# Kernel optimization log

Measured on AMD Instinct MI355X. Metric: run time of the kernel, lower is better.

Reference implementation:

```python
import jax, jax.numpy as jnp
import numpy as np

B, S, D = 32, 257, 1024
H, HD = 16, 64
E, R, K = 8, 16, 2
SCALE = HD ** -0.5


def _lora_linear(x, w_fixed, A_all, B_all, bias, idx, gates):
    # x: [B,S,D]; w_fixed: [O,D]; A_all: [E,R,D]; B_all: [E,O,R]; idx: [B,K]; gates: [B,K]
    base = jnp.einsum('bsd,od->bso', x, w_fixed)
    A_sel = A_all[idx]  # [B,K,R,D] per-sample expert gather
    B_sel = B_all[idx]  # [B,K,O,R]
    xa = jnp.einsum('bsd,bkrd->bksr', x, A_sel)          # low-rank down-proj
    expert = jnp.einsum('bksr,bkor,bk->bso', xa, B_sel, gates)
    return base + expert + bias


def setup_inputs() -> dict:
    key = jax.random.key(0)
    ks = jax.random.split(key, 20)
    inp = {
        'hidden_states': jax.random.normal(ks[0], (B, S, D), jnp.float32),
        'top_k_indices': jax.random.randint(ks[1], (B, K), 0, E),
        'top_k_gates': jax.random.uniform(ks[2], (B, K), jnp.float32),
    }
    i = 3
    for name in ('q', 'k', 'v', 'o'):
        inp[f'w{name}_fixed'] = jax.random.normal(ks[i], (D, D), jnp.float32) * 0.02; i += 1
        inp[f'A_{name}'] = jax.random.normal(ks[i], (E, R, D), jnp.float32) * 0.02; i += 1
        inp[f'B_{name}'] = jax.random.normal(ks[i], (E, D, R), jnp.float32) * 0.02; i += 1
        inp[f'b_{name}'] = jnp.zeros((D,), jnp.float32)
    return inp


def reference(hidden_states, top_k_indices, top_k_gates,
              wq_fixed, A_q, B_q, b_q,
              wk_fixed, A_k, B_k, b_k,
              wv_fixed, A_v, B_v, b_v,
              wo_fixed, A_o, B_o, b_o):
    idx, gates = top_k_indices, top_k_gates
    q = _lora_linear(hidden_states, wq_fixed, A_q, B_q, b_q, idx, gates) * SCALE
    k = _lora_linear(hidden_states, wk_fixed, A_k, B_k, b_k, idx, gates)
    v = _lora_linear(hidden_states, wv_fixed, A_v, B_v, b_v, idx, gates)
    # [B,S,D] -> [B,H,S,HD]
    q = q.reshape(B, S, H, HD).transpose(0, 2, 1, 3)
    k = k.reshape(B, S, H, HD).transpose(0, 2, 1, 3)
    v = v.reshape(B, S, H, HD).transpose(0, 2, 1, 3)
    attn = jax.nn.softmax(jnp.einsum('bhsd,bhtd->bhst', q, k), axis=-1)
    out = jnp.einsum('bhst,bhtd->bhsd', attn, v)
    out = out.transpose(0, 2, 1, 3).reshape(B, S, D)
    return _lora_linear(out, wo_fixed, A_o, B_o, b_o, idx, gates)
```

## Files before the change

### kernel.cpp

```cpp
#include <hip/hip_runtime.h>


#define BB 32
#define SS 257
#define DD 1024
#define HH 16
#define HDIM 64
#define EE 8
#define RR 16
#define MTOT (BB * SS)
#define MPAD 8320
#define VTS 264

typedef __attribute__((ext_vector_type(8))) _Float16 f16x8;
typedef __attribute__((ext_vector_type(4))) float f32x4;

static __device__ __forceinline__ float4 ld4(const float* p) {
    return *(const float4*)p;
}
static __device__ __forceinline__ unsigned short f16b(float x) {
    union { _Float16 f; unsigned short u; } cv;
    cv.f = (_Float16)x;
    return cv.u;
}

static __device__ __forceinline__ void gl_lds16(const unsigned short* g,
                                                unsigned short* l) {
    __builtin_amdgcn_global_load_lds(
        (const __attribute__((address_space(1))) unsigned int*)g,
        (__attribute__((address_space(3))) unsigned int*)l, 16, 0, 0);
}

__global__ __launch_bounds__(256) void prep(
    const float* __restrict__ hidden, const float* __restrict__ wq,
    const float* __restrict__ wk, const float* __restrict__ wv,
    const float* __restrict__ wo, const float* __restrict__ Aq,
    const float* __restrict__ Ak, const float* __restrict__ Av,
    const float* __restrict__ Ao, const float* __restrict__ Bq,
    const float* __restrict__ Bk, const float* __restrict__ Bv,
    const float* __restrict__ Bo, const int* __restrict__ tki,
    const float* __restrict__ tkg, unsigned short* __restrict__ Xf,
    unsigned short* __restrict__ Wcat, unsigned short* __restrict__ Who,
    unsigned short* __restrict__ A3, unsigned short* __restrict__ Ao16,
    unsigned short* __restrict__ Bccat, unsigned short* __restrict__ Bco)
{
    const int tid = threadIdx.x;
    int bx = blockIdx.x;
    if (bx < 8320) {
        long i = ((long)bx * 256 + tid) * 4;
        float4 v = (i < (long)MTOT * DD) ? ld4(&hidden[i])
                                         : make_float4(0.f, 0.f, 0.f, 0.f);
        ushort4 hv;
        hv.x = f16b(v.x); hv.y = f16b(v.y); hv.z = f16b(v.z); hv.w = f16b(v.w);
        *(ushort4*)&Xf[i] = hv;
        return;
    }
    bx -= 8320;
    if (bx < 4096) {
        const int sel = bx >> 10;
        long i = ((long)(bx & 1023) * 256 + tid) * 4;
        const float* src = (sel == 0) ? wq : (sel == 1) ? wk
                                          : (sel == 2) ? wv : wo;
        unsigned short* dst =
            (sel < 3) ? Wcat + (size_t)sel * DD * DD : Who;
        float4 v = ld4(&src[i]);
        ushort4 hv;
        hv.x = f16b(v.x); hv.y = f16b(v.y); hv.z = f16b(v.z); hv.w = f16b(v.w);
        *(ushort4*)&dst[i] = hv;
        return;
    }
    bx -= 4096;
    if (bx < 512) {
        const int sel = bx >> 7;
        long i = ((long)(bx & 127) * 256 + tid) * 4;
        const float* src = (sel == 0) ? Aq : (sel == 1) ? Ak
                                          : (sel == 2) ? Av : Ao;
        unsigned short* dst =
            (sel < 3) ? A3 + (size_t)sel * EE * RR * DD : Ao16;
        float4 v = ld4(&src[i]);
        ushort4 hv;
        hv.x = f16b(v.x); hv.y = f16b(v.y); hv.z = f16b(v.z); hv.w = f16b(v.w);
        *(ushort4*)&dst[i] = hv;
        return;
    }
    bx -= 512;
    {
        const int set = bx >> 8;
        const int i = (bx & 255) * 256 + tid;
        const int b = i >> 11;
        const int rem = i & 2047;
        const int n = rem >> 1;
        const int ke = rem & 1;
        const float* Ball = (set == 0) ? Bq : (set == 1) ? Bk
                                           : (set == 2) ? Bv : Bo;
        const int e = tki[b * 2 + ke];
        const float g = tkg[b * 2 + ke];
        const float* sp = &Ball[((size_t)e * DD + n) * RR];
        unsigned short o16[16];
#pragma unroll
        for (int r4 = 0; r4 < 4; ++r4) {
            float4 v = ld4(sp + r4 * 4);
            o16[r4 * 4 + 0] = f16b(g * v.x);
            o16[r4 * 4 + 1] = f16b(g * v.y);
            o16[r4 * 4 + 2] = f16b(g * v.z);
            o16[r4 * 4 + 3] = f16b(g * v.w);
        }
        unsigned short* dst =
            (set < 3) ? &Bccat[((size_t)b * 3072 + set * 1024 + n) * 32 + ke * 16]
                      : &Bco[((size_t)b * 1024 + n) * 32 + ke * 16];
        *(uint4*)&dst[0] = *(uint4*)&o16[0];
        *(uint4*)&dst[8] = *(uint4*)&o16[8];
    }
}

#define COMPUTE1()                                                             \
    do {                                                                       \
        f16x8 af[4], bf[4];                                                    \
        const int sb = (quad ^ ((l16 >> 1) & 3)) * 8;                          \
        _Pragma("unroll") for (int t = 0; t < 4; ++t) {                        \
            af[t] = *(const f16x8*)&Ah[(wm + t * 16 + l16) * 32 + sb];         \
            bf[t] = *(const f16x8*)&Bh[(wn + t * 16 + l16) * 32 + sb];         \
        }                                                                      \
        _Pragma("unroll") for (int i = 0; i < 4; ++i)                          \
        _Pragma("unroll") for (int j = 0; j < 4; ++j)                          \
            acc[i][j] = __builtin_amdgcn_mfma_f32_16x16x32_f16(                \
                af[i], bf[j], acc[i][j], 0, 0, 0);                             \
    } while (0)

__global__ __launch_bounds__(256) void gemm_xa(
    const unsigned short* __restrict__ Xf, const unsigned short* __restrict__ A0,
    const unsigned short* __restrict__ A1, const unsigned short* __restrict__ A2,
    unsigned short* __restrict__ XA, int ncols)
{
    __shared__ unsigned short Ah[128 * 32];
    __shared__ unsigned short Bh[128 * 32];
    const int tid = threadIdx.x;
    const int m0 = blockIdx.y * 128;
    const int p = blockIdx.x;
    const unsigned short* Ap = (p == 0) ? A0 : (p == 1) ? A1 : A2;
    const int lane = tid & 63;
    const int w = tid >> 6;
    const int wm = (w >> 1) * 64;
    const int wn = (w & 1) * 64;
    const int l16 = lane & 15;
    const int quad = lane >> 4;

    f32x4 acc[4][4];
#pragma unroll
    for (int i = 0; i < 4; ++i)
#pragma unroll
        for (int j = 0; j < 4; ++j) acc[i][j] = (f32x4){0.f, 0.f, 0.f, 0.f};

    const int srow = tid >> 2;
    const int scol = (((tid & 3) ^ ((tid >> 3) & 3))) * 8;
    const int lbase = (tid & 192) * 8;
    const size_t xr0 = (size_t)(m0 + srow) * DD + scol;
    const size_t xr1 = (size_t)(m0 + srow + 64) * DD + scol;
    const size_t ar0 = (size_t)srow * DD + scol;
    const size_t ar1 = (size_t)(srow + 64) * DD + scol;

#pragma unroll 1
    for (int kt = 0; kt < 32; ++kt) {
        const int k0 = kt * 32;
        gl_lds16(Xf + xr0 + k0, &Ah[lbase]);
        gl_lds16(Xf + xr1 + k0, &Ah[2048 + lbase]);
        gl_lds16(Ap + ar0 + k0, &Bh[lbase]);
        gl_lds16(Ap + ar1 + k0, &Bh[2048 + lbase]);
        __syncthreads();
        COMPUTE1();
        __syncthreads();
    }

#pragma unroll
    for (int j = 0; j < 4; ++j) {
        const int col = p * 128 + wn + j * 16 + l16;
#pragma unroll
        for (int i = 0; i < 4; ++i) {
            const int mb = m0 + wm + i * 16 + quad * 4;
#pragma unroll
            for (int rg = 0; rg < 4; ++rg) {
                const int m = mb + rg;
                if (m < MTOT)
                    XA[(size_t)m * ncols + col] = f16b(acc[i][j][rg]);
            }
        }
    }
}

__global__ __launch_bounds__(256) void gemm_qkv(
    const unsigned short* __restrict__ Xf, const unsigned short* __restrict__ Wcat,
    const float* __restrict__ bq, const float* __restrict__ bk,
    const float* __restrict__ bv, const unsigned short* __restrict__ XAd,
    const unsigned short* __restrict__ Bccat, const int* __restrict__ idx,
    unsigned short* __restrict__ qh, unsigned short* __restrict__ kh,
    unsigned short* __restrict__ vTg)
{
    __shared__ unsigned short Ah[128 * 32];
    __shared__ unsigned short Bh[128 * 32];
    __shared__ unsigned short Epi[8704];
    const int tid = threadIdx.x;
    const int m0 = blockIdx.y * 128;
    const int bx = blockIdx.x;
    const int p = bx >> 3;
    const int n0g = bx * 128;
    const int nl0 = (bx & 7) * 128;
    const int lane = tid & 63;
    const int w = tid >> 6;
    const int wm = (w >> 1) * 64;
    const int wn = (w & 1) * 64;
    const int l16 = lane & 15;
    const int quad = lane >> 4;

    f32x4 acc[4][4];
#pragma unroll
    for (int i = 0; i < 4; ++i)
#pragma unroll
        for (int j = 0; j < 4; ++j) acc[i][j] = (f32x4){0.f, 0.f, 0.f, 0.f};

    const int srow = tid >> 2;
    const int scol = (((tid & 3) ^ ((tid >> 3) & 3))) * 8;
    const int lbase = (tid & 192) * 8;
    const size_t xr0 = (size_t)(m0 + srow) * DD + scol;
    const size_t xr1 = (size_t)(m0 + srow + 64) * DD + scol;
    const size_t wr0 = (size_t)(n0g + srow) * DD + scol;
    const size_t wr1 = (size_t)(n0g + srow + 64) * DD + scol;

#pragma unroll 1
    for (int kt = 0; kt < 32; ++kt) {
        const int k0 = kt * 32;
        gl_lds16(Xf + xr0 + k0, &Ah[lbase]);
        gl_lds16(Xf + xr1 + k0, &Ah[2048 + lbase]);
        gl_lds16(Wcat + wr0 + k0, &Bh[lbase]);
        gl_lds16(Wcat + wr1 + k0, &Bh[2048 + lbase]);
        __syncthreads();
        COMPUTE1();
        __syncthreads();
    }

    {
        int m_hi = m0 + 127;
        if (m_hi >= MTOT) m_hi = MTOT - 1;
        const int b_first = m0 / SS;
        const int b_last = m_hi / SS;
        const int r = tid >> 1;
        const int key = (r >> 1) & 3;
        const int b0 = (tid & 1) * 2;
        const uint4 z = make_uint4(0, 0, 0, 0);
#pragma unroll 1
        for (int bp = b_first; bp <= b_last; ++bp) {
            const int gm = m0 + r;
            const bool va = (gm < MTOT) && (gm / SS == bp);
            const int g0 = b0 ^ key, g1 = (b0 + 1) ^ key;
            uint4 av0 = z, av1 = z;
            if (va) {
                const int e0 = idx[bp * 2 + (g0 >> 1)];
                const int e1 = idx[bp * 2 + (g1 >> 1)];
                av0 = *(const uint4*)&XAd[(size_t)gm * 384 + p * 128 +
                                          e0 * 16 + (g0 & 1) * 8];
                av1 = *(const uint4*)&XAd[(size_t)gm * 384 + p * 128 +
                                          e1 * 16 + (g1 & 1) * 8];
            }
            const size_t bo = ((size_t)bp * 3072 + p * 1024 + nl0 + r) * 32;
            uint4 bv0 = *(const uint4*)&Bccat[bo + g0 * 8];
            uint4 bv1 = *(const uint4*)&Bccat[bo + g1 * 8];
            __syncthreads();
            *(uint4*)&Ah[r * 32 + b0 * 8] = av0;
            *(uint4*)&Ah[r * 32 + (b0 + 1) * 8] = av1;
            *(uint4*)&Bh[r * 32 + b0 * 8] = bv0;
            *(uint4*)&Bh[r * 32 + (b0 + 1) * 8] = bv1;
            __syncthreads();
            COMPUTE1();
            __syncthreads();
        }
    }

    const float* bias = (p == 0) ? bq : (p == 1) ? bk : bv;
    if (p < 2) {
        const float alpha = (p == 0) ? 0.125f : 1.0f;
        unsigned short* C = (p == 0) ? qh : kh;
#pragma unroll 1
        for (int half = 0; half < 2; ++half) {
            if ((w >> 1) == half) {
#pragma unroll
                for (int j = 0; j < 4; ++j) {
                    const int nl = wn + j * 16 + l16;
                    const float bvl = bias[nl0 + nl];
#pragma unroll
                    for (int i = 0; i < 4; ++i) {
                        const int ml = i * 16 + quad * 4;
#pragma unroll
                        for (int rg = 0; rg < 4; ++rg)
                            Epi[(ml + rg) * 136 + nl] =
                                f16b(alpha * (acc[i][j][rg] + bvl));
                    }
                }
            }
            __syncthreads();
            {
                const int r = tid >> 2;
                const int c = (tid & 3) * 32;
                const int m = m0 + half * 64 + r;
                if (m < MTOT) {
#pragma unroll
                    for (int k = 0; k < 4; ++k)
                        *(uint4*)&C[(size_t)m * DD + nl0 + c + k * 8] =
                            *(const uint4*)&Epi[r * 136 + c + k * 8];
                }
            }
            __syncthreads();
        }
    } else {
#pragma unroll 1
        for (int half = 0; half < 2; ++half) {
            if ((w >> 1) == half) {
#pragma unroll
                for (int j = 0; j < 4; ++j) {
                    const int nl = wn + j * 16 + l16;
                    const float bvl = bias[nl0 + nl];
#pragma unroll
                    for (int i = 0; i < 4; ++i) {
                        const int ml = i * 16 + quad * 4;
                        ushort4 pk;
                        pk.x = f16b(acc[i][j][0] + bvl);
                        pk.y = f16b(acc[i][j][1] + bvl);
                        pk.z = f16b(acc[i][j][2] + bvl);
                        pk.w = f16b(acc[i][j][3] + bvl);
                        *(ushort4*)&Epi[nl * 68 + ml] = pk;
                    }
                }
            }
            __syncthreads();
            {
                const int tl = tid & 63;
                const int mg = m0 + half * 64 + tl;
                if (mg < MTOT) {
                    const int bq2 = mg / SS;
                    const int t = mg - bq2 * SS;
#pragma unroll 4
                    for (int k = 0; k < 32; ++k) {
                        const int nll = (tid >> 6) + k * 4;
                        const int d = nl0 + nll;
                        vTg[((size_t)(bq2 * HH + (d >> 6)) * HDIM + (d & 63)) *
                                VTS + t] = Epi[nll * 68 + tl];
                    }
                }
            }
            __syncthreads();
        }
    }
}

__global__ __launch_bounds__(256) void gemm_o(
    const unsigned short* __restrict__ Xf, const unsigned short* __restrict__ Wh2,
    const float* __restrict__ bias, const unsigned short* __restrict__ XAo,
    const unsigned short* __restrict__ Bco, const int* __restrict__ idx,
    float* __restrict__ Cf)
{
    __shared__ unsigned short Ah[128 * 32];
    __shared__ unsigned short Bh[128 * 32];
    const int tid = threadIdx.x;
    const int m0 = blockIdx.y * 128;
    const int n0 = blockIdx.x * 128;
    const int lane = tid & 63;
    const int w = tid >> 6;
    const int wm = (w >> 1) * 64;
    const int wn = (w & 1) * 64;
    const int l16 = lane & 15;
    const int quad = lane >> 4;

    f32x4 acc[4][4];
#pragma unroll
    for (int i = 0; i < 4; ++i)
#pragma unroll
        for (int j = 0; j < 4; ++j) acc[i][j] = (f32x4){0.f, 0.f, 0.f, 0.f};

    const int srow = tid >> 2;
    const int scol = (((tid & 3) ^ ((tid >> 3) & 3))) * 8;
    const int lbase = (tid & 192) * 8;
    const size_t xr0 = (size_t)(m0 + srow) * DD + scol;
    const size_t xr1 = (size_t)(m0 + srow + 64) * DD + scol;
    const size_t wr0 = (size_t)(n0 + srow) * DD + scol;
    const size_t wr1 = (size_t)(n0 + srow + 64) * DD + scol;

#pragma unroll 1
    for (int kt = 0; kt < 32; ++kt) {
        const int k0 = kt * 32;
        gl_lds16(Xf + xr0 + k0, &Ah[lbase]);
        gl_lds16(Xf + xr1 + k0, &Ah[2048 + lbase]);
        gl_lds16(Wh2 + wr0 + k0, &Bh[lbase]);
        gl_lds16(Wh2 + wr1 + k0, &Bh[2048 + lbase]);
        __syncthreads();
        COMPUTE1();
        __syncthreads();
    }

    {
        int m_hi = m0 + 127;
        if (m_hi >= MTOT) m_hi = MTOT - 1;
        const int b_first = m0 / SS;
        const int b_last = m_hi / SS;
        const int r = tid >> 1;
        const int key = (r >> 1) & 3;
        const int b0 = (tid & 1) * 2;
        const uint4 z = make_uint4(0, 0, 0, 0);
#pragma unroll 1
        for (int bp = b_first; bp <= b_last; ++bp) {
            const int gm = m0 + r;
            const bool va = (gm < MTOT) && (gm / SS == bp);
            const int g0 = b0 ^ key, g1 = (b0 + 1) ^ key;
            uint4 av0 = z, av1 = z;
            if (va) {
                const int e0 = idx[bp * 2 + (g0 >> 1)];
                const int e1 = idx[bp * 2 + (g1 >> 1)];
                av0 = *(const uint4*)&XAo[(size_t)gm * 128 + e0 * 16 +
                                          (g0 & 1) * 8];
                av1 = *(const uint4*)&XAo[(size_t)gm * 128 + e1 * 16 +
                                          (g1 & 1) * 8];
            }
            const size_t bo = ((size_t)bp * 1024 + n0 + r) * 32;
            uint4 bv0 = *(const uint4*)&Bco[bo + g0 * 8];
            uint4 bv1 = *(const uint4*)&Bco[bo + g1 * 8];
            __syncthreads();
            *(uint4*)&Ah[r * 32 + b0 * 8] = av0;
            *(uint4*)&Ah[r * 32 + (b0 + 1) * 8] = av1;
            *(uint4*)&Bh[r * 32 + b0 * 8] = bv0;
            *(uint4*)&Bh[r * 32 + (b0 + 1) * 8] = bv1;
            __syncthreads();
            COMPUTE1();
            __syncthreads();
        }
    }

#pragma unroll
    for (int j = 0; j < 4; ++j) {
        const int n = n0 + wn + j * 16 + l16;
        const float bvl = bias[n];
#pragma unroll
        for (int i = 0; i < 4; ++i) {
            const int mb = m0 + wm + i * 16 + quad * 4;
#pragma unroll
            for (int rg = 0; rg < 4; ++rg) {
                const int m = mb + rg;
                if (m < MTOT) Cf[(size_t)m * DD + n] = acc[i][j][rg] + bvl;
            }
        }
    }
}

__global__ __launch_bounds__(512, 1) void attn_v4(
    const unsigned short* __restrict__ qh, const unsigned short* __restrict__ kh,
    const unsigned short* __restrict__ vT, unsigned short* __restrict__ Xf)
{
    __shared__ unsigned short Ks[288 * 64];
    __shared__ unsigned short Vt[64 * VTS];
    __shared__ unsigned short Qs[64 * 64];
    __shared__ unsigned short Ps[64 * 296];
    __shared__ float sredm[2][64];
    __shared__ float sreds[2][64];

    const int tid = threadIdx.x;
    const int h = blockIdx.x, b = blockIdx.y;
    const int cb = h * HDIM;
    const int lane = tid & 63;
    const int w = tid >> 6;
    const int r0 = (w & 3) * 16;
    const int ch = w >> 2;
    const int l16 = lane & 15;
    const int quad = lane >> 4;

    const size_t kbase = (size_t)(b * SS) * DD + cb;
    {
        const int rr = w * 8 + (lane >> 3);
        const int cg = ((lane & 7) ^ (rr & 7)) * 8;
#pragma unroll
        for (int c = 0; c < 4; ++c)
            gl_lds16(kh + kbase + (size_t)(c * 64 + rr) * DD + cg,
                     &Ks[(c * 64 + w * 8) * 64]);
    }
    if (tid < 256) {
        uint4 z = make_uint4(0, 0, 0, 0);
        if (tid < 8) z = *(const uint4*)&kh[kbase + (size_t)256 * DD + tid * 8];
        *(uint4*)&Ks[256 * 64 + tid * 8] = z;
    }
    {
        const size_t vbase = (size_t)(b * HH + h) * HDIM * VTS;
        for (int i = tid; i < 64 * 33; i += 512) {
            const int r = i / 33;
            const int c = i - r * 33;
            uint4 v = *(const uint4*)&vT[vbase + (size_t)r * VTS + c * 8];
            if (c == 32) { v.x &= 0xFFFFu; v.y = 0; v.z = 0; v.w = 0; }
            *(uint4*)&Vt[r * VTS + c * 8] = v;
        }
    }

#pragma unroll 1
    for (int qt = 0; qt < 5; ++qt) {
        const int s0 = qt * 64;
        __syncthreads();
        {
            int sg = s0 + (tid >> 3);
            if (sg > SS - 1) sg = SS - 1;
            const int cg = ((tid & 7) ^ ((tid >> 3) & 7)) * 8;
            gl_lds16(qh + (size_t)(b * SS + sg) * DD + cb + cg,
                     &Qs[(w * 8) * 64]);
        }
        __syncthreads();

        f32x4 lac[9];
#pragma unroll
        for (int ct = 0; ct < 9; ++ct) lac[ct] = (f32x4){0.f, 0.f, 0.f, 0.f};
#pragma unroll
        for (int kc = 0; kc < 2; ++kc) {
            const int sb = ((kc * 4 + quad) ^ (l16 & 7)) * 8;
            f16x8 af = *(const f16x8*)&Qs[(r0 + l16) * 64 + sb];
#pragma unroll
            for (int ct = 0; ct < 9; ++ct) {
                const int c0 = ch * 144 + ct * 16;
                f16x8 bf = *(const f16x8*)&Ks[(c0 + l16) * 64 + sb];
                lac[ct] = __builtin_amdgcn_mfma_f32_16x16x32_f16(
                    af, bf, lac[ct], 0, 0, 0);
            }
        }
#pragma unroll
        for (int ct = 0; ct < 9; ++ct) {
            const int t = ch * 144 + ct * 16 + l16;
            if (t > SS - 1) {
                lac[ct][0] = -1e30f; lac[ct][1] = -1e30f;
                lac[ct][2] = -1e30f; lac[ct][3] = -1e30f;
            }
        }
        float mx[4] = {-1e30f, -1e30f, -1e30f, -1e30f};
#pragma unroll
        for (int ct = 0; ct < 9; ++ct)
#pragma unroll
            for (int i = 0; i < 4; ++i) mx[i] = fmaxf(mx[i], lac[ct][i]);
#pragma unroll
        for (int o = 1; o < 16; o <<= 1)
#pragma unroll
            for (int i = 0; i < 4; ++i)
                mx[i] = fmaxf(mx[i], __shfl_xor(mx[i], o, 16));
        if (l16 == 0)
#pragma unroll
            for (int i = 0; i < 4; ++i) sredm[ch][r0 + quad * 4 + i] = mx[i];
        __syncthreads();
#pragma unroll
        for (int i = 0; i < 4; ++i)
            mx[i] = fmaxf(mx[i], sredm[1 - ch][r0 + quad * 4 + i]);
        float sm[4] = {0.f, 0.f, 0.f, 0.f};
#pragma unroll
        for (int ct = 0; ct < 9; ++ct)
#pragma unroll
            for (int i = 0; i < 4; ++i) {
                float pv = __expf(lac[ct][i] - mx[i]);
                lac[ct][i] = pv;
                sm[i] += pv;
            }
#pragma unroll
        for (int o = 1; o < 16; o <<= 1)
#pragma unroll
            for (int i = 0; i < 4; ++i) sm[i] += __shfl_xor(sm[i], o, 16);
        if (l16 == 0)
#pragma unroll
            for (int i = 0; i < 4; ++i) sreds[ch][r0 + quad * 4 + i] = sm[i];
        __syncthreads();
        float inv[4];
#pragma unroll
        for (int i = 0; i < 4; ++i)
            inv[i] = 1.f / (sm[i] + sreds[1 - ch][r0 + quad * 4 + i]);
#pragma unroll
        for (int ct = 0; ct < 9; ++ct) {
            const int col = ch * 144 + ct * 16 + l16;
#pragma unroll
            for (int i = 0; i < 4; ++i)
                Ps[(r0 + quad * 4 + i) * 296 + col] =
                    f16b(lac[ct][i] * inv[i]);
        }
        __syncthreads();

        f32x4 oacc[2];
        oacc[0] = (f32x4){0.f, 0.f, 0.f, 0.f};
        oacc[1] = (f32x4){0.f, 0.f, 0.f, 0.f};
#pragma unroll
        for (int tt = 0; tt < 9; ++tt) {
            const int t0 = tt * 32;
            f16x8 pf = *(const f16x8*)&Ps[(r0 + l16) * 296 + t0 + quad * 8];
#pragma unroll
            for (int dt = 0; dt < 2; ++dt) {
                f16x8 bvv = *(const f16x8*)&Vt[(ch * 32 + dt * 16 + l16) * VTS +
                                               t0 + quad * 8];
                oacc[dt] = __builtin_amdgcn_mfma_f32_16x16x32_f16(
                    pf, bvv, oacc[dt], 0, 0, 0);
            }
        }
#pragma unroll
        for (int dt = 0; dt < 2; ++dt)
#pragma unroll
            for (int i = 0; i < 4; ++i) {
                const int srow = s0 + r0 + quad * 4 + i;
                if (srow < SS)
                    Xf[(size_t)(b * SS + srow) * DD + cb + ch * 32 + dt * 16 +
                       l16] = f16b(oacc[dt][i]);
            }
    }
}

extern "C" void kernel_launch(void* const* d_in, const int* in_sizes, int n_in,
                              void* d_out, int out_size, void* d_ws,
                              size_t ws_size, hipStream_t stream)
{
    const float* hidden = (const float*)d_in[0];
    const int* tki = (const int*)d_in[1];
    const float* tkg = (const float*)d_in[2];
    const float* wq = (const float*)d_in[3];
    const float* Aq = (const float*)d_in[4];
    const float* Bq = (const float*)d_in[5];
    const float* bq = (const float*)d_in[6];
    const float* wk = (const float*)d_in[7];
    const float* Ak = (const float*)d_in[8];
    const float* Bk = (const float*)d_in[9];
    const float* bkb = (const float*)d_in[10];
    const float* wv = (const float*)d_in[11];
    const float* Av = (const float*)d_in[12];
    const float* Bv = (const float*)d_in[13];
    const float* bvb = (const float*)d_in[14];
    const float* wo = (const float*)d_in[15];
    const float* Ao = (const float*)d_in[16];
    const float* Bo = (const float*)d_in[17];
    const float* bob = (const float*)d_in[18];
    float* out = (float*)d_out;

    char* ws = (char*)d_ws;
    const size_t NW = (size_t)DD * DD;
    const size_t NA = (size_t)EE * RR * DD;
    unsigned short* Xf = (unsigned short*)ws;    ws += (size_t)MPAD * DD * 2;
    unsigned short* qh = (unsigned short*)ws;    ws += (size_t)MTOT * DD * 2;
    unsigned short* vTg = (unsigned short*)ws;   ws += (size_t)BB * HH * HDIM * VTS * 2;
    unsigned short* Wcat = (unsigned short*)ws;  ws += 3 * NW * 2;
    unsigned short* Who = (unsigned short*)ws;   ws += NW * 2;
    unsigned short* A3 = (unsigned short*)ws;    ws += 3 * NA * 2;
    unsigned short* Ao16 = (unsigned short*)ws;  ws += NA * 2;
    unsigned short* Bccat = (unsigned short*)ws; ws += (size_t)BB * 3072 * 32 * 2;
    unsigned short* Bco = (unsigned short*)ws;   ws += (size_t)BB * 1024 * 32 * 2;
    unsigned short* XAo = (unsigned short*)ws;   ws += (size_t)MTOT * 128 * 2;
    unsigned short* kh = (unsigned short*)d_out;
    unsigned short* XAd = (unsigned short*)((char*)d_out + (size_t)MTOT * DD * 2);

    prep<<<13952, 256, 0, stream>>>(hidden, wq, wk, wv, wo, Aq, Ak, Av, Ao,
                                    Bq, Bk, Bv, Bo, tki, tkg, Xf, Wcat, Who,
                                    A3, Ao16, Bccat, Bco);
    gemm_xa<<<dim3(3, 65), 256, 0, stream>>>(Xf, A3, A3 + NA, A3 + 2 * NA,
                                             XAd, 384);
    gemm_qkv<<<dim3(24, 65), 256, 0, stream>>>(Xf, Wcat, bq, bkb, bvb, XAd,
                                               Bccat, tki, qh, kh, vTg);
    attn_v4<<<dim3(HH, BB), 512, 0, stream>>>(qh, kh, vTg, Xf);
    gemm_xa<<<dim3(1, 65), 256, 0, stream>>>(Xf, Ao16, Ao16, Ao16, XAo, 128);
    gemm_o<<<dim3(8, 65), 256, 0, stream>>>(Xf, Who, bob, XAo, Bco, tki, out);
}
```

Before: 383.7 us.

## Enlarge QKV GEMM tile to 256x256 with a 4-stage async LDS pipeline

Reworks gemm_qkv to use 512-thread blocks computing 256x256 output tiles, each wave holding an 8x4 grid of MFMA accumulators. Global-to-LDS copies run through a four-buffer ring with explicit vmcnt waits and a single barrier per k-step, and s_setprio is raised around the MFMA bursts. This is meant to cut global traffic per FLOP and to overlap loads with compute. The cost is 128 KB of LDS and higher register pressure, so only one block fits per CU. The padded M size grows to 8448 so the larger tiles stay in bounds, and the LoRA and epilogue stages are adapted to the new tile shape.

```diff
diff --git a/kernel.cpp b/kernel.cpp
--- a/kernel.cpp
+++ b/kernel.cpp
@@ -9,7 +9,7 @@
 #define EE 8
 #define RR 16
 #define MTOT (BB * SS)
-#define MPAD 8320
+#define MPAD 8448
 #define VTS 264
 
 typedef __attribute__((ext_vector_type(8))) _Float16 f16x8;
@@ -46,7 +46,7 @@
 {
     const int tid = threadIdx.x;
     int bx = blockIdx.x;
-    if (bx < 8320) {
+    if (bx < 8448) {
         long i = ((long)bx * 256 + tid) * 4;
         float4 v = (i < (long)MTOT * DD) ? ld4(&hidden[i])
                                          : make_float4(0.f, 0.f, 0.f, 0.f);
@@ -55,7 +55,7 @@
         *(ushort4*)&Xf[i] = hv;
         return;
     }
-    bx -= 8320;
+    bx -= 8448;
     if (bx < 4096) {
         const int sel = bx >> 10;
         long i = ((long)(bx & 1023) * 256 + tid) * 4;
@@ -187,7 +187,42 @@
     }
 }
 
-__global__ __launch_bounds__(256) void gemm_qkv(
+#define QKV_STAGE(BUFI, KT)                                                    \
+    do {                                                                       \
+        unsigned short* dA_ = S + (BUFI) * 16384 + w * 512;                    \
+        const int k0_ = (KT) * 32;                                             \
+        gl_lds16(Xf + gA + k0_, dA_);                                          \
+        gl_lds16(Xf + gA + 128 * DD + k0_, dA_ + 4096);                        \
+        gl_lds16(Wcat + gB + k0_, dA_ + 8192);                                 \
+        gl_lds16(Wcat + gB + 128 * DD + k0_, dA_ + 12288);                     \
+    } while (0)
+
+#define QKV_PHASES(BUFI)                                                       \
+    do {                                                                       \
+        const unsigned short* Ab_ = S + (BUFI) * 16384;                        \
+        const unsigned short* Bb_ = Ab_ + 8192;                                \
+        f16x8 bf_[4], af_[4];                                                  \
+        _Pragma("unroll") for (int j = 0; j < 4; ++j)                          \
+            bf_[j] = *(const f16x8*)&Bb_[boff + j * 512];                      \
+        _Pragma("unroll") for (int i = 0; i < 4; ++i)                          \
+            af_[i] = *(const f16x8*)&Ab_[aoff + i * 512];                      \
+        __builtin_amdgcn_s_setprio(1);                                         \
+        _Pragma("unroll") for (int i = 0; i < 4; ++i)                          \
+        _Pragma("unroll") for (int j = 0; j < 4; ++j)                          \
+            acc[i][j] = __builtin_amdgcn_mfma_f32_16x16x32_f16(                \
+                af_[i], bf_[j], acc[i][j], 0, 0, 0);                           \
+        __builtin_amdgcn_s_setprio(0);                                         \
+        _Pragma("unroll") for (int i = 0; i < 4; ++i)                          \
+            af_[i] = *(const f16x8*)&Ab_[aoff + 2048 + i * 512];               \
+        __builtin_amdgcn_s_setprio(1);                                         \
+        _Pragma("unroll") for (int i = 0; i < 4; ++i)                          \
+        _Pragma("unroll") for (int j = 0; j < 4; ++j)                          \
+            acc[i + 4][j] = __builtin_amdgcn_mfma_f32_16x16x32_f16(            \
+                af_[i], bf_[j], acc[i + 4][j], 0, 0, 0);                       \
+        __builtin_amdgcn_s_setprio(0);                                         \
+    } while (0)
+
+__global__ __launch_bounds__(512) void gemm_qkv(
     const unsigned short* __restrict__ Xf, const unsigned short* __restrict__ Wcat,
     const float* __restrict__ bq, const float* __restrict__ bk,
     const float* __restrict__ bv, const unsigned short* __restrict__ XAd,
@@ -195,50 +230,50 @@
     unsigned short* __restrict__ qh, unsigned short* __restrict__ kh,
     unsigned short* __restrict__ vTg)
 {
-    __shared__ unsigned short Ah[128 * 32];
-    __shared__ unsigned short Bh[128 * 32];
-    __shared__ unsigned short Epi[8704];
+    __shared__ unsigned short S[65536];
     const int tid = threadIdx.x;
-    const int m0 = blockIdx.y * 128;
-    const int bx = blockIdx.x;
-    const int p = bx >> 3;
-    const int n0g = bx * 128;
-    const int nl0 = (bx & 7) * 128;
+    const int bxn = blockIdx.x;
+    const int m0 = blockIdx.y * 256;
+    const int p = bxn >> 2;
+    const int n0g = bxn * 256;
+    const int nloc0 = (bxn & 3) * 256;
     const int lane = tid & 63;
     const int w = tid >> 6;
-    const int wm = (w >> 1) * 64;
-    const int wn = (w & 1) * 64;
+    const int wm = (w >> 2) * 128;
+    const int wn = (w & 3) * 64;
     const int l16 = lane & 15;
     const int quad = lane >> 4;
-
-    f32x4 acc[4][4];
-#pragma unroll
-    for (int i = 0; i < 4; ++i)
+    const int sb = (quad ^ ((l16 >> 1) & 3)) * 8;
+    const int aoff = (wm + l16) * 32 + sb;
+    const int boff = (wn + l16) * 32 + sb;
+
+    f32x4 acc[8][4];
+#pragma unroll
+    for (int i = 0; i < 8; ++i)
 #pragma unroll
         for (int j = 0; j < 4; ++j) acc[i][j] = (f32x4){0.f, 0.f, 0.f, 0.f};
 
-    const int srow = tid >> 2;
-    const int scol = (((tid & 3) ^ ((tid >> 3) & 3))) * 8;
-    const int lbase = (tid & 192) * 8;
-    const size_t xr0 = (size_t)(m0 + srow) * DD + scol;
-    const size_t xr1 = (size_t)(m0 + srow + 64) * DD + scol;
-    const size_t wr0 = (size_t)(n0g + srow) * DD + scol;
-    const size_t wr1 = (size_t)(n0g + srow + 64) * DD + scol;
-
-#pragma unroll 1
-    for (int kt = 0; kt < 32; ++kt) {
-        const int k0 = kt * 32;
-        gl_lds16(Xf + xr0 + k0, &Ah[lbase]);
-        gl_lds16(Xf + xr1 + k0, &Ah[2048 + lbase]);
-        gl_lds16(Wcat + wr0 + k0, &Bh[lbase]);
-        gl_lds16(Wcat + wr1 + k0, &Bh[2048 + lbase]);
-        __syncthreads();
-        COMPUTE1();
-        __syncthreads();
-    }
+    const int srow = w * 16 + (lane >> 2);
+    const int schk = ((lane & 3) ^ ((srow >> 1) & 3)) * 8;
+    const size_t gA = (size_t)(m0 + srow) * DD + schk;
+    const size_t gB = (size_t)(n0g + srow) * DD + schk;
+
+    QKV_STAGE(0, 0);
+    QKV_STAGE(1, 1);
+    QKV_STAGE(2, 2);
+#pragma unroll 1
+    for (int kt = 0; kt < 30; ++kt) {
+        asm volatile("s_waitcnt vmcnt(8)\n\ts_barrier" ::: "memory");
+        if (kt < 29) QKV_STAGE((kt + 3) & 3, kt + 3);
+        QKV_PHASES(kt & 3);
+    }
+    asm volatile("s_waitcnt vmcnt(4)\n\ts_barrier" ::: "memory");
+    QKV_PHASES(2);
+    asm volatile("s_waitcnt vmcnt(0)\n\ts_barrier" ::: "memory");
+    QKV_PHASES(3);
 
     {
-        int m_hi = m0 + 127;
+        int m_hi = m0 + 255;
         if (m_hi >= MTOT) m_hi = MTOT - 1;
         const int b_first = m0 / SS;
         const int b_last = m_hi / SS;
@@ -260,37 +295,38 @@
                 av1 = *(const uint4*)&XAd[(size_t)gm * 384 + p * 128 +
                                           e1 * 16 + (g1 & 1) * 8];
             }
-            const size_t bo = ((size_t)bp * 3072 + p * 1024 + nl0 + r) * 32;
+            const size_t bo = ((size_t)bp * 3072 + p * 1024 + nloc0 + r) * 32;
             uint4 bv0 = *(const uint4*)&Bccat[bo + g0 * 8];
             uint4 bv1 = *(const uint4*)&Bccat[bo + g1 * 8];
             __syncthreads();
-            *(uint4*)&Ah[r * 32 + b0 * 8] = av0;
-            *(uint4*)&Ah[r * 32 + (b0 + 1) * 8] = av1;
-            *(uint4*)&Bh[r * 32 + b0 * 8] = bv0;
-            *(uint4*)&Bh[r * 32 + (b0 + 1) * 8] = bv1;
-            __syncthreads();
-            COMPUTE1();
-            __syncthreads();
-        }
-    }
-
+            *(uint4*)&S[r * 32 + b0 * 8] = av0;
+            *(uint4*)&S[r * 32 + (b0 + 1) * 8] = av1;
+            *(uint4*)&S[8192 + r * 32 + b0 * 8] = bv0;
+            *(uint4*)&S[8192 + r * 32 + (b0 + 1) * 8] = bv1;
+            __syncthreads();
+            QKV_PHASES(0);
+            __syncthreads();
+        }
+    }
+
+    unsigned short* Epi = S;
     const float* bias = (p == 0) ? bq : (p == 1) ? bk : bv;
     if (p < 2) {
         const float alpha = (p == 0) ? 0.125f : 1.0f;
         unsigned short* C = (p == 0) ? qh : kh;
 #pragma unroll 1
         for (int half = 0; half < 2; ++half) {
-            if ((w >> 1) == half) {
+            if ((w >> 2) == half) {
 #pragma unroll
                 for (int j = 0; j < 4; ++j) {
-                    const int nl = wn + j * 16 + l16;
-                    const float bvl = bias[nl0 + nl];
-#pragma unroll
-                    for (int i = 0; i < 4; ++i) {
+                    const int col = wn + j * 16 + l16;
+                    const float bvl = bias[nloc0 + col];
+#pragma unroll
+                    for (int i = 0; i < 8; ++i) {
                         const int ml = i * 16 + quad * 4;
 #pragma unroll
                         for (int rg = 0; rg < 4; ++rg)
-                            Epi[(ml + rg) * 136 + nl] =
+                            Epi[(ml + rg) * 264 + col] =
                                 f16b(alpha * (acc[i][j][rg] + bvl));
                     }
                 }
@@ -298,48 +334,49 @@
             __syncthreads();
             {
                 const int r = tid >> 2;
-                const int c = (tid & 3) * 32;
-                const int m = m0 + half * 64 + r;
+                const int c = (tid & 3) * 64;
+                const int m = m0 + half * 128 + r;
                 if (m < MTOT) {
 #pragma unroll
-                    for (int k = 0; k < 4; ++k)
-                        *(uint4*)&C[(size_t)m * DD + nl0 + c + k * 8] =
-                            *(const uint4*)&Epi[r * 136 + c + k * 8];
+                    for (int k = 0; k < 8; ++k)
+                        *(uint4*)&C[(size_t)m * DD + nloc0 + c + k * 8] =
+                            *(const uint4*)&Epi[r * 264 + c + k * 8];
                 }
             }
             __syncthreads();
         }
     } else {
 #pragma unroll 1
-        for (int half = 0; half < 2; ++half) {
-            if ((w >> 1) == half) {
+        for (int hh = 0; hh < 4; ++hh) {
+            if ((w >> 2) == (hh >> 1)) {
 #pragma unroll
                 for (int j = 0; j < 4; ++j) {
-                    const int nl = wn + j * 16 + l16;
-                    const float bvl = bias[nl0 + nl];
-#pragma unroll
-                    for (int i = 0; i < 4; ++i) {
-                        const int ml = i * 16 + quad * 4;
+                    const int col = wn + j * 16 + l16;
+                    const float bvl = bias[nloc0 + col];
+#pragma unroll
+                    for (int i2 = 0; i2 < 4; ++i2) {
+                        const int i = (hh & 1) * 4 + i2;
+                        const int ml = i2 * 16 + quad * 4;
                         ushort4 pk;
                         pk.x = f16b(acc[i][j][0] + bvl);
                         pk.y = f16b(acc[i][j][1] + bvl);
                         pk.z = f16b(acc[i][j][2] + bvl);
                         pk.w = f16b(acc[i][j][3] + bvl);
-                        *(ushort4*)&Epi[nl * 68 + ml] = pk;
+                        *(ushort4*)&Epi[col * 68 + ml] = pk;
                     }
                 }
             }
             __syncthreads();
             {
                 const int tl = tid & 63;
-                const int mg = m0 + half * 64 + tl;
+                const int mg = m0 + hh * 64 + tl;
                 if (mg < MTOT) {
                     const int bq2 = mg / SS;
                     const int t = mg - bq2 * SS;
 #pragma unroll 4
                     for (int k = 0; k < 32; ++k) {
-                        const int nll = (tid >> 6) + k * 4;
-                        const int d = nl0 + nll;
+                        const int nll = (tid >> 6) + k * 8;
+                        const int d = nloc0 + nll;
                         vTg[((size_t)(bq2 * HH + (d >> 6)) * HDIM + (d & 63)) *
                                 VTS + t] = Epi[nll * 68 + tl];
                     }
@@ -645,12 +682,12 @@
     unsigned short* kh = (unsigned short*)d_out;
     unsigned short* XAd = (unsigned short*)((char*)d_out + (size_t)MTOT * DD * 2);
 
-    prep<<<13952, 256, 0, stream>>>(hidden, wq, wk, wv, wo, Aq, Ak, Av, Ao,
+    prep<<<14080, 256, 0, stream>>>(hidden, wq, wk, wv, wo, Aq, Ak, Av, Ao,
                                     Bq, Bk, Bv, Bo, tki, tkg, Xf, Wcat, Who,
                                     A3, Ao16, Bccat, Bco);
     gemm_xa<<<dim3(3, 65), 256, 0, stream>>>(Xf, A3, A3 + NA, A3 + 2 * NA,
                                              XAd, 384);
-    gemm_qkv<<<dim3(24, 65), 256, 0, stream>>>(Xf, Wcat, bq, bkb, bvb, XAd,
+    gemm_qkv<<<dim3(12, 33), 512, 0, stream>>>(Xf, Wcat, bq, bkb, bvb, XAd,
                                                Bccat, tki, qh, kh, vTg);
     attn_v4<<<dim3(HH, BB), 512, 0, stream>>>(qh, kh, vTg, Xf);
     gemm_xa<<<dim3(1, 65), 256, 0, stream>>>(Xf, Ao16, Ao16, Ao16, XAo, 128);
```

Measured after the change: 444.2 us. 15.8% more time.
